# Optimization experiments

Measured on AMD Instinct MI355X. Metric: run time of the kernel, lower is better.

Reference implementation:

```python
import jax, jax.numpy as jnp
import numpy as np

B, L, D = 8, 4096, 512  # batch, seq_len (power of 2), in_features
R_MIN, R_MAX = 0.9, 0.999


def setup_inputs() -> dict:
    key = jax.random.key(0)
    k1, k2, k3 = jax.random.split(key, 3)
    inputs = jax.random.normal(k1, (B, L, D), dtype=jnp.float32)
    # Linear layers: i_dense D->2D, o_dense 2D->D (torch Linear: y = x @ W.T + b)
    Wi = jax.random.normal(k2, (2 * D, D), dtype=jnp.float32) / np.sqrt(D)
    bi = jnp.zeros((2 * D,), dtype=jnp.float32)
    Wo = jax.random.normal(k3, (D, 2 * D), dtype=jnp.float32) / np.sqrt(2 * D)
    bo = jnp.zeros((D,), dtype=jnp.float32)
    # LRU param init, exactly as in the torch module
    rng = np.random.RandomState(0)
    u1 = rng.random_sample(D)
    u2 = rng.random_sample(D)
    v_log = np.log(-0.5 * np.log(u1 * (R_MAX ** 2 - R_MIN ** 2) + R_MIN ** 2))
    theta_log = np.log(u2 * np.pi * 2)
    gamma_log = np.log(np.sqrt(1 - np.exp(-np.exp(v_log)) ** 2))
    params_log = jnp.asarray(np.stack([v_log, theta_log, gamma_log]), dtype=jnp.float32)
    return {"inputs": inputs, "Wi": Wi, "bi": bi, "Wo": Wo, "bo": bo,
            "params_log": params_log}


def reference(inputs, Wi, bi, Wo, bo, params_log):
    b, lin, d = inputs.shape
    u = inputs @ Wi.T + bi                       # [B, L, 2D]
    params = jnp.exp(params_log)                 # [3, D]
    v, theta, gamma = params[0], params[1], params[2]
    log2_L = int(np.ceil(np.log2(lin)))
    Lp = 2 ** log2_L
    # interleaved (real, imag) pairs -> complex state
    u = u.reshape(b, lin, d, 2)
    x = jax.lax.complex(u[..., 0], u[..., 1])    # [B, L, D] complex64
    if Lp > lin:
        x = jnp.pad(x, ((0, 0), (0, Lp - lin), (0, 0)))
    # Blelloch-style doubling scan: after stage i, each block of length 2^i
    # holds the prefix-scanned values x_t = lam*x_{t-1} + u_t within the block.
    for i in range(1, log2_L + 1):
        l = 2 ** i
        xr = x.reshape(b * Lp // l, l, d)
        x1, x2 = xr[:, : l // 2], xr[:, l // 2 :]
        pos = jnp.arange(1, l // 2 + 1, dtype=jnp.float32)        # [l/2]
        lambs = jnp.exp(jax.lax.complex(-pos[:, None] * v,
                                        pos[:, None] * theta))   # [l/2, D]
        x2 = x2 + lambs * x1[:, -1:]
        x = jnp.concatenate([x1, x2], axis=1).reshape(b, Lp, d)
    x = x[:, :lin] * gamma.astype(jnp.complex64)
    xr = jnp.concatenate([jnp.real(x), jnp.imag(x)], axis=-1)     # [B, L, 2D]
    out = xr @ Wo.T + bo
    return jax.nn.relu(out)
```

## Files before the change

### kernel.cpp

```cpp
#include <hip/hip_runtime.h>
#include <cstdint>
#include <cstddef>

typedef unsigned short u16;
typedef unsigned int   u32;

typedef short bf16x8 __attribute__((ext_vector_type(8)));
typedef float f32x4  __attribute__((ext_vector_type(4)));

__device__ __forceinline__ u16 f2bf(float f) {
  u32 u = __float_as_uint(f);
  u += 0x7fffu + ((u >> 16) & 1u);
  return (u16)(u >> 16);
}
__device__ __forceinline__ float bflo(u32 w) { return __uint_as_float((w & 0xffffu) << 16); }
__device__ __forceinline__ float bfhi(u32 w) { return __uint_as_float(w & 0xffff0000u); }

#define GLB_AS(p) ((const __attribute__((address_space(1))) void*)(p))
#define LDS_AS(p) ((__attribute__((address_space(3))) void*)(p))

__global__ __launch_bounds__(256)
void conv3_f32_bf16(const float* __restrict__ in, u16* __restrict__ a,
                    const float* __restrict__ wi, u16* __restrict__ wib,
                    const float* __restrict__ wo, u16* __restrict__ wob)
{
  long i = (long)blockIdx.x * 256 + threadIdx.x;
  const float* src; u16* dst;
  if (i < 4194304L) { src = in; dst = a; }
  else if (i < 4325376L) { i -= 4194304L; src = wi; dst = wib; }
  else { i -= 4325376L; if (i >= 131072L) return; src = wo; dst = wob; }
  float4 v = ((const float4*)src)[i];
  u32 lo = (u32)f2bf(v.x) | ((u32)f2bf(v.y) << 16);
  u32 hi = (u32)f2bf(v.z) | ((u32)f2bf(v.w) << 16);
  ((uint2*)dst)[i] = make_uint2(lo, hi);
}

template<int N, int K, int LOGNB, int OUT_BF16, int RELU>
__global__ __launch_bounds__(512, 4)
void gemm_w2(const u16* __restrict__ A, const u16* __restrict__ Bw,
             const float* __restrict__ bias, void* __restrict__ Cout)
{
  __shared__ __align__(16) u16 As[3][256 * 32];
  __shared__ __align__(16) u16 Bs[3][128 * 32];

  const int tid  = threadIdx.x;
  const int lane = tid & 63;
  const int wave = tid >> 6;
  const int bid  = blockIdx.x;
  const int xcd  = bid & 7;
  const int s    = bid >> 3;
  const int m0 = (xcd * 16 + (s >> LOGNB)) * 256;
  const int n0 = (s & ((1 << LOGNB) - 1)) * 128;
  const int wm = (wave & 3) * 64;
  const int wn = (wave >> 2) * 64;

  f32x4 acc[4][4];
#pragma unroll
  for (int i = 0; i < 4; ++i)
#pragma unroll
    for (int j = 0; j < 4; ++j) acc[i][j] = f32x4{0.f, 0.f, 0.f, 0.f};

  const u16* Ap[2]; const u16* Bp; int ldsA[2]; int ldsB;
#pragma unroll
  for (int i = 0; i < 2; ++i) {
    int g = i * 512 + tid;
    int r = g >> 2;
    int koff = ((g & 3) ^ ((r >> 1) & 3)) << 3;
    Ap[i]   = A + (size_t)(m0 + r) * K + koff;
    ldsA[i] = (i * 512 + wave * 64) * 8;
  }
  {
    int g = tid;
    int r = g >> 2;
    int koff = ((g & 3) ^ ((r >> 1) & 3)) << 3;
    Bp   = Bw + (size_t)(n0 + r) * K + koff;
    ldsB = (wave * 64) * 8;
  }

  const int fm = lane & 15;
  const int q  = lane >> 4;
  int aoff[4], boff[4];
#pragma unroll
  for (int i = 0; i < 4; ++i) {
    int m = wm + i * 16 + fm;
    aoff[i] = (m * 4 + (q ^ ((m >> 1) & 3))) * 8;
    int n = wn + i * 16 + fm;
    boff[i] = (n * 4 + (q ^ ((n >> 1) & 3))) * 8;
  }

  auto stage = [&](int buf, int kt) {
    __builtin_amdgcn_global_load_lds(GLB_AS(Ap[0] + kt), LDS_AS(&As[buf][ldsA[0]]), 16, 0, 0);
    __builtin_amdgcn_global_load_lds(GLB_AS(Ap[1] + kt), LDS_AS(&As[buf][ldsA[1]]), 16, 0, 0);
    __builtin_amdgcn_global_load_lds(GLB_AS(Bp    + kt), LDS_AS(&Bs[buf][ldsB]),    16, 0, 0);
  };
  auto compute = [&](int buf) {
    bf16x8 af[4], bfr[4];
#pragma unroll
    for (int i = 0; i < 4; ++i) { af[i]  = *(const bf16x8*)&As[buf][aoff[i]];
                                  bfr[i] = *(const bf16x8*)&Bs[buf][boff[i]]; }
#pragma unroll
    for (int mi = 0; mi < 4; ++mi)
#pragma unroll
      for (int ni = 0; ni < 4; ++ni)
        acc[mi][ni] = __builtin_amdgcn_mfma_f32_16x16x32_bf16(af[mi], bfr[ni],
                                                              acc[mi][ni], 0, 0, 0);
  };

  constexpr int NT = K / 32;
  stage(0, 0);
  stage(1, 32);
#pragma unroll
  for (int t = 0; t < NT - 1; ++t) {
    asm volatile("s_waitcnt vmcnt(3)" ::: "memory");
    __builtin_amdgcn_s_barrier();
    if (t + 2 < NT) stage((t + 2) % 3, (t + 2) * 32);
    compute(t % 3);
  }
  asm volatile("s_waitcnt vmcnt(0)" ::: "memory");
  __builtin_amdgcn_s_barrier();
  compute((NT - 1) % 3);

  const int colL = lane & 15;
  const int rowQ = (lane >> 4) * 4;
#pragma unroll
  for (int mi = 0; mi < 4; ++mi) {
#pragma unroll
    for (int ni = 0; ni < 4; ++ni) {
      int col  = n0 + wn + ni * 16 + colL;
      int rowb = m0 + wm + mi * 16 + rowQ;
      float bv = bias[col];
#pragma unroll
      for (int r = 0; r < 4; ++r) {
        float v = acc[mi][ni][r] + bv;
        if (RELU) v = fmaxf(v, 0.f);
        size_t idx = (size_t)(rowb + r) * N + col;
        if (OUT_BF16) ((u16*)Cout)[idx] = f2bf(v);
        else          ((float*)Cout)[idx] = v;
      }
    }
  }
}

__global__ __launch_bounds__(256)
void scan_chunk_end(const u16* __restrict__ u, const float* __restrict__ plog,
                    float4* __restrict__ e)
{
  const int t  = threadIdx.x;
  const int tt = t & 127;
  const int c  = blockIdx.x * 2 + (t >> 7);
  const int b  = blockIdx.y;
  float4 vl = ((const float4*)plog)[tt];
  float4 tl = ((const float4*)plog)[128 + tt];
  float vlog[4] = {vl.x, vl.y, vl.z, vl.w};
  float tlog[4] = {tl.x, tl.y, tl.z, tl.w};
  float lr[4], li[4], hr[4], hi4[4];
#pragma unroll
  for (int k = 0; k < 4; ++k) {
    float v  = expf(vlog[k]);
    float th = expf(tlog[k]);
    float mg = expf(-v);
    lr[k] = mg * cosf(th); li[k] = mg * sinf(th);
    hr[k] = 0.f; hi4[k] = 0.f;
  }
  const uint4* up = (const uint4*)u;
  size_t idx = (size_t)(b * 4096 + c * 32) * 128 + tt;
#pragma unroll 8
  for (int s = 0; s < 32; ++s) {
    uint4 w = up[idx]; idx += 128;
    u32 ws[4] = {w.x, w.y, w.z, w.w};
#pragma unroll
    for (int k = 0; k < 4; ++k) {
      float ur = bflo(ws[k]), ui = bfhi(ws[k]);
      float nr = fmaf(lr[k], hr[k], fmaf(-li[k], hi4[k], ur));
      float ni = fmaf(lr[k], hi4[k], fmaf( li[k], hr[k], ui));
      hr[k] = nr; hi4[k] = ni;
    }
  }
  size_t eb = (size_t)(b * 128 + c) * 256 + 2 * tt;
  e[eb]     = make_float4(hr[0], hi4[0], hr[1], hi4[1]);
  e[eb + 1] = make_float4(hr[2], hi4[2], hr[3], hi4[3]);
}

__global__ __launch_bounds__(256)
void scan_out2(const u16* __restrict__ u, const float* __restrict__ plog,
               const float4* __restrict__ e, u16* __restrict__ xr)
{
  const int t  = threadIdx.x;
  const int tt = t & 127;
  const int c  = blockIdx.x * 2 + (t >> 7);
  const int b  = blockIdx.y;
  float4 vl = ((const float4*)plog)[tt];
  float4 tl = ((const float4*)plog)[128 + tt];
  float4 gl = ((const float4*)plog)[256 + tt];
  float vlog[4] = {vl.x, vl.y, vl.z, vl.w};
  float tlog[4] = {tl.x, tl.y, tl.z, tl.w};
  float glog[4] = {gl.x, gl.y, gl.z, gl.w};
  float lr[4], li[4], Lr[4], Li[4], gm[4], hr[4], hi4[4];
#pragma unroll
  for (int k = 0; k < 4; ++k) {
    float v  = expf(vlog[k]);
    float th = expf(tlog[k]);
    gm[k] = expf(glog[k]);
    float mg = expf(-v);
    lr[k] = mg * cosf(th); li[k] = mg * sinf(th);
    float Lm = expf(-32.f * v);
    float La = 32.f * th;
    Lr[k] = Lm * cosf(La); Li[k] = Lm * sinf(La);
    hr[k] = 0.f; hi4[k] = 0.f;
  }

  size_t ebase = (size_t)(b * 128) * 256 + 2 * tt;
#pragma unroll 4
  for (int i = 0; i < c; ++i) {
    float4 e0 = e[ebase + (size_t)i * 256];
    float4 e1 = e[ebase + (size_t)i * 256 + 1];
    float n0r = fmaf(Lr[0], hr[0], fmaf(-Li[0], hi4[0], e0.x));
    float n0i = fmaf(Lr[0], hi4[0], fmaf( Li[0], hr[0], e0.y));
    float n1r = fmaf(Lr[1], hr[1], fmaf(-Li[1], hi4[1], e0.z));
    float n1i = fmaf(Lr[1], hi4[1], fmaf( Li[1], hr[1], e0.w));
    float n2r = fmaf(Lr[2], hr[2], fmaf(-Li[2], hi4[2], e1.x));
    float n2i = fmaf(Lr[2], hi4[2], fmaf( Li[2], hr[2], e1.y));
    float n3r = fmaf(Lr[3], hr[3], fmaf(-Li[3], hi4[3], e1.z));
    float n3i = fmaf(Lr[3], hi4[3], fmaf( Li[3], hr[3], e1.w));
    hr[0] = n0r; hi4[0] = n0i; hr[1] = n1r; hi4[1] = n1i;
    hr[2] = n2r; hi4[2] = n2i; hr[3] = n3r; hi4[3] = n3i;
  }

  const uint4* up = (const uint4*)u;
  uint2* xp = (uint2*)xr;
  size_t uidx = (size_t)(b * 4096 + c * 32) * 128 + tt;
  size_t xidx = (size_t)(b * 4096 + c * 32) * 256 + tt;
#pragma unroll 8
  for (int s2 = 0; s2 < 32; ++s2) {
    uint4 w = up[uidx]; uidx += 128;
    u32 ws[4] = {w.x, w.y, w.z, w.w};
#pragma unroll
    for (int k = 0; k < 4; ++k) {
      float ur = bflo(ws[k]), ui = bfhi(ws[k]);
      float nr = fmaf(lr[k], hr[k], fmaf(-li[k], hi4[k], ur));
      float ni = fmaf(lr[k], hi4[k], fmaf( li[k], hr[k], ui));
      hr[k] = nr; hi4[k] = ni;
    }
    u32 re0 = (u32)f2bf(gm[0] * hr[0])  | ((u32)f2bf(gm[1] * hr[1])  << 16);
    u32 re1 = (u32)f2bf(gm[2] * hr[2])  | ((u32)f2bf(gm[3] * hr[3])  << 16);
    u32 im0 = (u32)f2bf(gm[0] * hi4[0]) | ((u32)f2bf(gm[1] * hi4[1]) << 16);
    u32 im1 = (u32)f2bf(gm[2] * hi4[2]) | ((u32)f2bf(gm[3] * hi4[3]) << 16);
    xp[xidx]       = make_uint2(re0, re1);
    xp[xidx + 128] = make_uint2(im0, im1);
    xidx += 256;
  }
}

extern "C" void kernel_launch(void* const* d_in, const int* in_sizes, int n_in,
                              void* d_out, int out_size, void* d_ws, size_t ws_size,
                              hipStream_t stream)
{
  (void)in_sizes; (void)n_in; (void)out_size; (void)ws_size;
  const float* inputs = (const float*)d_in[0];
  const float* Wi     = (const float*)d_in[1];
  const float* bi     = (const float*)d_in[2];
  const float* Wo     = (const float*)d_in[3];
  const float* bo     = (const float*)d_in[4];
  const float* plog   = (const float*)d_in[5];

  char* ws = (char*)d_ws;
  u16*    xrA   = (u16*)(ws);
  u16*    u_bf  = (u16*)(ws + 67108864ull);
  u16*    Wi_bf = (u16*)(ws + 134217728ull);
  u16*    Wo_bf = (u16*)(ws + 135266304ull);
  float4* e_b   = (float4*)(ws + 136314880ull);

  conv3_f32_bf16<<<17408, 256, 0, stream>>>(inputs, xrA, Wi, Wi_bf, Wo, Wo_bf);

  gemm_w2<1024, 512, 3, 1, 0><<<1024, 512, 0, stream>>>(xrA, Wi_bf, bi, u_bf);

  scan_chunk_end<<<dim3(64, 8), 256, 0, stream>>>(u_bf, plog, e_b);
  scan_out2<<<dim3(64, 8), 256, 0, stream>>>(u_bf, plog, e_b, xrA);

  gemm_w2<512, 1024, 2, 0, 1><<<512, 512, 0, stream>>>(xrA, Wo_bf, bo, d_out);
}
```

Before: 251.9 us.

## Enlarge GEMM tiles to 256x256 and add serial chunk-carry scan kernel

After: 290.5 us. +15.3%, slower.

```diff
diff --git a/kernel.cpp b/kernel.cpp
--- a/kernel.cpp
+++ b/kernel.cpp
@@ -36,12 +36,12 @@
 }
 
 template<int N, int K, int LOGNB, int OUT_BF16, int RELU>
-__global__ __launch_bounds__(512, 4)
+__global__ __launch_bounds__(512, 2)
 void gemm_w2(const u16* __restrict__ A, const u16* __restrict__ Bw,
              const float* __restrict__ bias, void* __restrict__ Cout)
 {
   __shared__ __align__(16) u16 As[3][256 * 32];
-  __shared__ __align__(16) u16 Bs[3][128 * 32];
+  __shared__ __align__(16) u16 Bs[3][256 * 32];
 
   const int tid  = threadIdx.x;
   const int lane = tid & 63;
@@ -50,40 +50,37 @@
   const int xcd  = bid & 7;
   const int s    = bid >> 3;
   const int m0 = (xcd * 16 + (s >> LOGNB)) * 256;
-  const int n0 = (s & ((1 << LOGNB) - 1)) * 128;
+  const int n0 = (s & ((1 << LOGNB) - 1)) * 256;
   const int wm = (wave & 3) * 64;
-  const int wn = (wave >> 2) * 64;
-
-  f32x4 acc[4][4];
+  const int wn = (wave >> 2) * 128;
+
+  f32x4 acc[4][8];
 #pragma unroll
   for (int i = 0; i < 4; ++i)
 #pragma unroll
-    for (int j = 0; j < 4; ++j) acc[i][j] = f32x4{0.f, 0.f, 0.f, 0.f};
-
-  const u16* Ap[2]; const u16* Bp; int ldsA[2]; int ldsB;
+    for (int j = 0; j < 8; ++j) acc[i][j] = f32x4{0.f, 0.f, 0.f, 0.f};
+
+  const u16* Ap[2]; const u16* Bp[2]; int ldsA[2];
 #pragma unroll
   for (int i = 0; i < 2; ++i) {
     int g = i * 512 + tid;
     int r = g >> 2;
     int koff = ((g & 3) ^ ((r >> 1) & 3)) << 3;
-    Ap[i]   = A + (size_t)(m0 + r) * K + koff;
+    Ap[i]   = A  + (size_t)(m0 + r) * K + koff;
+    Bp[i]   = Bw + (size_t)(n0 + r) * K + koff;
     ldsA[i] = (i * 512 + wave * 64) * 8;
-  }
-  {
-    int g = tid;
-    int r = g >> 2;
-    int koff = ((g & 3) ^ ((r >> 1) & 3)) << 3;
-    Bp   = Bw + (size_t)(n0 + r) * K + koff;
-    ldsB = (wave * 64) * 8;
   }
 
   const int fm = lane & 15;
   const int q  = lane >> 4;
-  int aoff[4], boff[4];
+  int aoff[4], boff[8];
 #pragma unroll
   for (int i = 0; i < 4; ++i) {
     int m = wm + i * 16 + fm;
     aoff[i] = (m * 4 + (q ^ ((m >> 1) & 3))) * 8;
+  }
+#pragma unroll
+  for (int i = 0; i < 8; ++i) {
     int n = wn + i * 16 + fm;
     boff[i] = (n * 4 + (q ^ ((n >> 1) & 3))) * 8;
   }
@@ -91,17 +88,19 @@
   auto stage = [&](int buf, int kt) {
     __builtin_amdgcn_global_load_lds(GLB_AS(Ap[0] + kt), LDS_AS(&As[buf][ldsA[0]]), 16, 0, 0);
     __builtin_amdgcn_global_load_lds(GLB_AS(Ap[1] + kt), LDS_AS(&As[buf][ldsA[1]]), 16, 0, 0);
-    __builtin_amdgcn_global_load_lds(GLB_AS(Bp    + kt), LDS_AS(&Bs[buf][ldsB]),    16, 0, 0);
+    __builtin_amdgcn_global_load_lds(GLB_AS(Bp[0] + kt), LDS_AS(&Bs[buf][ldsA[0]]), 16, 0, 0);
+    __builtin_amdgcn_global_load_lds(GLB_AS(Bp[1] + kt), LDS_AS(&Bs[buf][ldsA[1]]), 16, 0, 0);
   };
   auto compute = [&](int buf) {
-    bf16x8 af[4], bfr[4];
-#pragma unroll
-    for (int i = 0; i < 4; ++i) { af[i]  = *(const bf16x8*)&As[buf][aoff[i]];
-                                  bfr[i] = *(const bf16x8*)&Bs[buf][boff[i]]; }
+    bf16x8 af[4], bfr[8];
+#pragma unroll
+    for (int i = 0; i < 4; ++i) af[i]  = *(const bf16x8*)&As[buf][aoff[i]];
+#pragma unroll
+    for (int i = 0; i < 8; ++i) bfr[i] = *(const bf16x8*)&Bs[buf][boff[i]];
 #pragma unroll
     for (int mi = 0; mi < 4; ++mi)
 #pragma unroll
-      for (int ni = 0; ni < 4; ++ni)
+      for (int ni = 0; ni < 8; ++ni)
         acc[mi][ni] = __builtin_amdgcn_mfma_f32_16x16x32_bf16(af[mi], bfr[ni],
                                                               acc[mi][ni], 0, 0, 0);
   };
@@ -109,15 +108,16 @@
   constexpr int NT = K / 32;
   stage(0, 0);
   stage(1, 32);
-#pragma unroll
   for (int t = 0; t < NT - 1; ++t) {
-    asm volatile("s_waitcnt vmcnt(3)" ::: "memory");
+    asm volatile("s_waitcnt vmcnt(4)" ::: "memory");
     __builtin_amdgcn_s_barrier();
+    __builtin_amdgcn_sched_barrier(0);
     if (t + 2 < NT) stage((t + 2) % 3, (t + 2) * 32);
     compute(t % 3);
   }
   asm volatile("s_waitcnt vmcnt(0)" ::: "memory");
   __builtin_amdgcn_s_barrier();
+  __builtin_amdgcn_sched_barrier(0);
   compute((NT - 1) % 3);
 
   const int colL = lane & 15;
@@ -125,7 +125,7 @@
 #pragma unroll
   for (int mi = 0; mi < 4; ++mi) {
 #pragma unroll
-    for (int ni = 0; ni < 4; ++ni) {
+    for (int ni = 0; ni < 8; ++ni) {
       int col  = n0 + wn + ni * 16 + colL;
       int rowb = m0 + wm + mi * 16 + rowQ;
       float bv = bias[col];
@@ -179,6 +179,45 @@
   size_t eb = (size_t)(b * 128 + c) * 256 + 2 * tt;
   e[eb]     = make_float4(hr[0], hi4[0], hr[1], hi4[1]);
   e[eb + 1] = make_float4(hr[2], hi4[2], hr[3], hi4[3]);
+}
+
+__global__ __launch_bounds__(128)
+void scan_mid(const float* __restrict__ plog, float4* __restrict__ e)
+{
+  const int t = threadIdx.x;
+  const int b = blockIdx.x;
+  float4 vl = ((const float4*)plog)[t];
+  float4 tl = ((const float4*)plog)[128 + t];
+  float vlog[4] = {vl.x, vl.y, vl.z, vl.w};
+  float tlog[4] = {tl.x, tl.y, tl.z, tl.w};
+  float Lr[4], Li[4], hr[4], hi4[4];
+#pragma unroll
+  for (int k = 0; k < 4; ++k) {
+    float v  = expf(vlog[k]);
+    float th = expf(tlog[k]);
+    float Lm = expf(-32.f * v);
+    float La = 32.f * th;
+    Lr[k] = Lm * cosf(La); Li[k] = Lm * sinf(La);
+    hr[k] = 0.f; hi4[k] = 0.f;
+  }
+  size_t base = (size_t)(b * 128) * 256 + 2 * t;
+#pragma unroll 4
+  for (int c = 0; c < 128; ++c) {
+    float4 e0 = e[base + (size_t)c * 256];
+    float4 e1 = e[base + (size_t)c * 256 + 1];
+    float n0r = fmaf(Lr[0], hr[0], fmaf(-Li[0], hi4[0], e0.x));
+    float n0i = fmaf(Lr[0], hi4[0], fmaf( Li[0], hr[0], e0.y));
+    float n1r = fmaf(Lr[1], hr[1], fmaf(-Li[1], hi4[1], e0.z));
+    float n1i = fmaf(Lr[1], hi4[1], fmaf( Li[1], hr[1], e0.w));
+    float n2r = fmaf(Lr[2], hr[2], fmaf(-Li[2], hi4[2], e1.x));
+    float n2i = fmaf(Lr[2], hi4[2], fmaf( Li[2], hr[2], e1.y));
+    float n3r = fmaf(Lr[3], hr[3], fmaf(-Li[3], hi4[3], e1.z));
+    float n3i = fmaf(Lr[3], hi4[3], fmaf( Li[3], hr[3], e1.w));
+    hr[0] = n0r; hi4[0] = n0i; hr[1] = n1r; hi4[1] = n1i;
+    hr[2] = n2r; hi4[2] = n2i; hr[3] = n3r; hi4[3] = n3i;
+    e[base + (size_t)c * 256]     = make_float4(hr[0], hi4[0], hr[1], hi4[1]);
+    e[base + (size_t)c * 256 + 1] = make_float4(hr[2], hi4[2], hr[3], hi4[3]);
+  }
 }
 
 __global__ __launch_bounds__(256)
@@ -195,7 +234,7 @@
   float vlog[4] = {vl.x, vl.y, vl.z, vl.w};
   float tlog[4] = {tl.x, tl.y, tl.z, tl.w};
   float glog[4] = {gl.x, gl.y, gl.z, gl.w};
-  float lr[4], li[4], Lr[4], Li[4], gm[4], hr[4], hi4[4];
+  float lr[4], li[4], gm[4], hr[4], hi4[4];
 #pragma unroll
   for (int k = 0; k < 4; ++k) {
     float v  = expf(vlog[k]);
@@ -203,27 +242,15 @@
     gm[k] = expf(glog[k]);
     float mg = expf(-v);
     lr[k] = mg * cosf(th); li[k] = mg * sinf(th);
-    float Lm = expf(-32.f * v);
-    float La = 32.f * th;
-    Lr[k] = Lm * cosf(La); Li[k] = Lm * sinf(La);
     hr[k] = 0.f; hi4[k] = 0.f;
   }
 
-  size_t ebase = (size_t)(b * 128) * 256 + 2 * tt;
-#pragma unroll 4
-  for (int i = 0; i < c; ++i) {
-    float4 e0 = e[ebase + (size_t)i * 256];
-    float4 e1 = e[ebase + (size_t)i * 256 + 1];
-    float n0r = fmaf(Lr[0], hr[0], fmaf(-Li[0], hi4[0], e0.x));
-    float n0i = fmaf(Lr[0], hi4[0], fmaf( Li[0], hr[0], e0.y));
-    float n1r = fmaf(Lr[1], hr[1], fmaf(-Li[1], hi4[1], e0.z));
-    float n1i = fmaf(Lr[1], hi4[1], fmaf( Li[1], hr[1], e0.w));
-    float n2r = fmaf(Lr[2], hr[2], fmaf(-Li[2], hi4[2], e1.x));
-    float n2i = fmaf(Lr[2], hi4[2], fmaf( Li[2], hr[2], e1.y));
-    float n3r = fmaf(Lr[3], hr[3], fmaf(-Li[3], hi4[3], e1.z));
-    float n3i = fmaf(Lr[3], hi4[3], fmaf( Li[3], hr[3], e1.w));
-    hr[0] = n0r; hi4[0] = n0i; hr[1] = n1r; hi4[1] = n1i;
-    hr[2] = n2r; hi4[2] = n2i; hr[3] = n3r; hi4[3] = n3i;
+  if (c > 0) {
+    size_t eb = (size_t)(b * 128 + c - 1) * 256 + 2 * tt;
+    float4 e0 = e[eb];
+    float4 e1 = e[eb + 1];
+    hr[0] = e0.x; hi4[0] = e0.y; hr[1] = e0.z; hi4[1] = e0.w;
+    hr[2] = e1.x; hi4[2] = e1.y; hr[3] = e1.z; hi4[3] = e1.w;
   }
 
   const uint4* up = (const uint4*)u;
@@ -272,10 +299,11 @@
 
   conv3_f32_bf16<<<17408, 256, 0, stream>>>(inputs, xrA, Wi, Wi_bf, Wo, Wo_bf);
 
-  gemm_w2<1024, 512, 3, 1, 0><<<1024, 512, 0, stream>>>(xrA, Wi_bf, bi, u_bf);
+  gemm_w2<1024, 512, 2, 1, 0><<<512, 512, 0, stream>>>(xrA, Wi_bf, bi, u_bf);
 
   scan_chunk_end<<<dim3(64, 8), 256, 0, stream>>>(u_bf, plog, e_b);
+  scan_mid<<<8, 128, 0, stream>>>(plog, e_b);
   scan_out2<<<dim3(64, 8), 256, 0, stream>>>(u_bf, plog, e_b, xrA);
 
-  gemm_w2<512, 1024, 2, 0, 1><<<512, 512, 0, stream>>>(xrA, Wo_bf, bo, d_out);
-}
+  gemm_w2<512, 1024, 1, 0, 1><<<256, 512, 0, stream>>>(xrA, Wo_bf, bo, d_out);
+}
```
